# Kernel tuning notes

Hardware: AMD Instinct MI355X
Metric: run time of the kernel (lower is better)

Reference implementation:

```python
import jax, jax.numpy as jnp
import numpy as np

DIM = 1024
N_HEADS = 16
HEAD_DIM = DIM // N_HEADS
SCALE = HEAD_DIM ** (-0.5)


def setup_inputs() -> dict:
    key = jax.random.key(0)
    ks = jax.random.split(key, 5)
    B, N = 2, 2048
    x = jax.random.normal(ks[0], (B, N, DIM), dtype=jnp.float32)
    # torch nn.Linear weight layout: (out_features, in_features)
    qkv_w = jax.random.normal(ks[1], (3 * DIM, DIM), dtype=jnp.float32) * 0.02
    qkv_b = jax.random.normal(ks[2], (3 * DIM,), dtype=jnp.float32) * 0.02
    proj_w = jax.random.normal(ks[3], (DIM, DIM), dtype=jnp.float32) * 0.02
    proj_b = jax.random.normal(ks[4], (DIM,), dtype=jnp.float32) * 0.02
    return {"x": x, "qkv_w": qkv_w, "qkv_b": qkv_b, "proj_w": proj_w, "proj_b": proj_b}


def reference(x, qkv_w, qkv_b, proj_w, proj_b):
    B, N, C = x.shape
    # QKV projection: (B,N,C) -> (B,N,3C)
    qkv = jnp.einsum('bnc,oc->bno', x, qkv_w) + qkv_b
    # (B,N,3,H,Dh) -> (3,B,H,N,Dh)
    qkv = qkv.reshape(B, N, 3, N_HEADS, HEAD_DIM).transpose(2, 0, 3, 1, 4)
    q, k, v = qkv[0], qkv[1], qkv[2]
    attn = jnp.einsum('bhqd,bhkd->bhqk', q, k) * SCALE
    attn = jax.nn.softmax(attn, axis=-1)
    out = jnp.einsum('bhqk,bhkd->bhqd', attn, v)
    out = out.transpose(0, 2, 1, 3).reshape(B, N, C)  # concat heads
    out = jnp.einsum('bnc,oc->bno', out, proj_w) + proj_b
    return out
```

## Files before the change

kernel.cpp:

```cpp
#include <hip/hip_runtime.h>

#define DIM 1024
#define NHEADS 16
#define HD 64
#define NSEQ 2048
#define MROWS 4096
#define QKV_LD 3072

typedef __attribute__((ext_vector_type(8))) short short8;
typedef __attribute__((ext_vector_type(4))) short short4v;
typedef __attribute__((ext_vector_type(4))) float f32x4;

typedef __attribute__((address_space(1))) void gvoid_t;
typedef __attribute__((address_space(3))) void lvoid_t;

#if __has_builtin(__builtin_amdgcn_exp2f)
#define EXP2(x) __builtin_amdgcn_exp2f(x)
#else
#define EXP2(x) exp2f(x)
#endif

#if __has_builtin(__builtin_amdgcn_mfma_f32_16x16x16_bf16)
#define MFMA16(a, b, c) __builtin_amdgcn_mfma_f32_16x16x16_bf16(a, b, c, 0, 0, 0)
#elif __has_builtin(__builtin_amdgcn_mfma_f32_16x16x16bf16_1k)
#define MFMA16(a, b, c) __builtin_amdgcn_mfma_f32_16x16x16bf16_1k(a, b, c, 0, 0, 0)
#else
static __device__ __forceinline__ f32x4 mfma16_asm(short4v a, short4v b, f32x4 c) {
  __asm__("v_mfma_f32_16x16x16_bf16 %0, %1, %2, %0" : "+v"(c) : "v"(a), "v"(b));
  return c;
}
#define MFMA16(a, b, c) mfma16_asm(a, b, c)
#endif

#define EXP_SCALE 0.18033688011112042f

__device__ __forceinline__ unsigned short f2bf(float f) {
  unsigned int u = __builtin_bit_cast(unsigned int, f);
  u += 0x7FFFu + ((u >> 16) & 1u);
  return (unsigned short)(u >> 16);
}

__device__ __forceinline__ void gl_lds16(const void* g, void* l) {
  __builtin_amdgcn_global_load_lds((gvoid_t*)g, (lvoid_t*)l, 16, 0, 0);
}

__global__ __launch_bounds__(256) void cast_bf16_3(
    const float* __restrict__ x, const float* __restrict__ wq,
    const float* __restrict__ wp,
    unsigned short* __restrict__ xb, unsigned short* __restrict__ wqb,
    unsigned short* __restrict__ wpb)
{
  int g = blockIdx.x * 256 + threadIdx.x;
  const float* src;
  unsigned short* dst;
  if (g < 1048576)            { src = x  + (size_t)g * 4;              dst = xb  + (size_t)g * 4; }
  else if (g < 1048576 + 786432) { int t = g - 1048576; src = wq + (size_t)t * 4; dst = wqb + (size_t)t * 4; }
  else                        { int t = g - 1048576 - 786432; src = wp + (size_t)t * 4; dst = wpb + (size_t)t * 4; }
  float4 v = *(const float4*)src;
  ushort4 o;
  o.x = f2bf(v.x); o.y = f2bf(v.y); o.z = f2bf(v.z); o.w = f2bf(v.w);
  *(ushort4*)dst = o;
}

__global__ __launch_bounds__(256) void gemm_nt(
    const unsigned short* __restrict__ A,
    const unsigned short* __restrict__ Bw,
    const float* __restrict__ bias,
    int K, int mode,
    unsigned short* __restrict__ oq,
    unsigned short* __restrict__ ovt,
    float* __restrict__ of)
{
  __shared__ unsigned short As[128 * 32];
  __shared__ unsigned short Bs[128 * 32];

  const int tid  = threadIdx.x;
  const int wave = tid >> 6, lane = tid & 63;
  const int quad = lane >> 4, l15 = lane & 15;
  const int mblk = blockIdx.x * 128;
  const int nblk = blockIdx.y * 128;
  const int wrow = (wave >> 1) * 64, wcol = (wave & 1) * 64;

  f32x4 acc[4][4] = {};

  const int sr = lane >> 2;
  const int sq = (lane & 3) ^ (sr & 3);
  const unsigned short* aBase = A  + (size_t)(mblk + wave * 32 + sr) * K + sq * 8;
  const unsigned short* bBase = Bw + (size_t)(nblk + wave * 32 + sr) * K + sq * 8;

  for (int k0 = 0; k0 < K; k0 += 32) {
    __syncthreads();
    gl_lds16(aBase + k0,          As + (wave * 32) * 32);
    gl_lds16(aBase + 16 * K + k0, As + (wave * 32 + 16) * 32);
    gl_lds16(bBase + k0,          Bs + (wave * 32) * 32);
    gl_lds16(bBase + 16 * K + k0, Bs + (wave * 32 + 16) * 32);
    __syncthreads();

    short8 af[4], bf8[4];
#pragma unroll
    for (int mt = 0; mt < 4; ++mt) {
      int row = wrow + mt * 16 + l15;
      af[mt] = *(const short8*)(As + row * 32 + ((quad ^ (row & 3)) * 8));
    }
#pragma unroll
    for (int nt = 0; nt < 4; ++nt) {
      int row = wcol + nt * 16 + l15;
      bf8[nt] = *(const short8*)(Bs + row * 32 + ((quad ^ (row & 3)) * 8));
    }
#pragma unroll
    for (int mt = 0; mt < 4; ++mt)
#pragma unroll
      for (int nt = 0; nt < 4; ++nt)
        acc[mt][nt] = __builtin_amdgcn_mfma_f32_16x16x32_bf16(af[mt], bf8[nt], acc[mt][nt], 0, 0, 0);
  }

  float bv[4];
#pragma unroll
  for (int nt = 0; nt < 4; ++nt) bv[nt] = bias[nblk + wcol + nt * 16 + l15];

  if (mode == 0) {
#pragma unroll
    for (int mt = 0; mt < 4; ++mt) {
      int row0 = mblk + wrow + mt * 16 + quad * 4;
#pragma unroll
      for (int nt = 0; nt < 4; ++nt) {
        int col = nblk + wcol + nt * 16 + l15;
#pragma unroll
        for (int r = 0; r < 4; ++r)
          of[(size_t)(row0 + r) * DIM + col] = acc[mt][nt][r] + bv[nt];
      }
    }
  } else if (nblk < 2048) {
    const float qs = (nblk < 1024) ? EXP_SCALE : 1.0f;
#pragma unroll
    for (int mt = 0; mt < 4; ++mt) {
      int row0 = mblk + wrow + mt * 16 + quad * 4;
#pragma unroll
      for (int nt = 0; nt < 4; ++nt) {
        int col = nblk + wcol + nt * 16 + l15;
#pragma unroll
        for (int r = 0; r < 4; ++r)
          oq[(size_t)(row0 + r) * QKV_LD + col] = f2bf((acc[mt][nt][r] + bv[nt]) * qs);
      }
    }
  } else {
#pragma unroll
    for (int mt = 0; mt < 4; ++mt) {
      int row0 = mblk + wrow + mt * 16 + quad * 4;
      int n0 = row0 & (NSEQ - 1);
      int bb = row0 >> 11;
      int tt  = n0 >> 6;
      int kin = n0 & 63;
      int kt  = kin >> 4;
      int qv  = (kin >> 2) & 3;
#pragma unroll
      for (int nt = 0; nt < 4; ++nt) {
        int colr = (nblk - 2048) + wcol + nt * 16 + l15;
        int bh = bb * NHEADS + (colr >> 6);
        int d  = colr & 63;
        int dt = d >> 4, dl15 = d & 15;
        ushort4 pk;
        pk.x = f2bf(acc[mt][nt][0] + bv[nt]);
        pk.y = f2bf(acc[mt][nt][1] + bv[nt]);
        pk.z = f2bf(acc[mt][nt][2] + bv[nt]);
        pk.w = f2bf(acc[mt][nt][3] + bv[nt]);
        size_t off = (size_t)(bh * 32 + tt) * 4096 + kt * 1024 + (dt >> 1) * 512
                   + qv * 128 + dl15 * 8 + (dt & 1) * 4;
        *(ushort4*)(ovt + off) = pk;
      }
    }
  }
}

__global__ __launch_bounds__(256) void gemm_nt64(
    const unsigned short* __restrict__ A,
    const unsigned short* __restrict__ Bw,
    const float* __restrict__ bias,
    int K,
    float* __restrict__ of)
{
  __shared__ unsigned short As[64 * 32];
  __shared__ unsigned short Bs[128 * 32];

  const int tid  = threadIdx.x;
  const int wave = tid >> 6, lane = tid & 63;
  const int quad = lane >> 4, l15 = lane & 15;
  const int mblk = blockIdx.x * 64;
  const int nblk = blockIdx.y * 128;
  const int wrow = (wave >> 1) * 32, wcol = (wave & 1) * 64;

  f32x4 acc[2][4] = {};

  const int sr = lane >> 2;
  const int sq = (lane & 3) ^ (sr & 3);
  const unsigned short* aBase = A  + (size_t)(mblk + wave * 16 + sr) * K + sq * 8;
  const unsigned short* bBase = Bw + (size_t)(nblk + wave * 32 + sr) * K + sq * 8;

  for (int k0 = 0; k0 < K; k0 += 32) {
    __syncthreads();
    gl_lds16(aBase + k0,          As + (wave * 16) * 32);
    gl_lds16(bBase + k0,          Bs + (wave * 32) * 32);
    gl_lds16(bBase + 16 * K + k0, Bs + (wave * 32 + 16) * 32);
    __syncthreads();

    short8 af[2], bf8[4];
#pragma unroll
    for (int mt = 0; mt < 2; ++mt) {
      int row = wrow + mt * 16 + l15;
      af[mt] = *(const short8*)(As + row * 32 + ((quad ^ (row & 3)) * 8));
    }
#pragma unroll
    for (int nt = 0; nt < 4; ++nt) {
      int row = wcol + nt * 16 + l15;
      bf8[nt] = *(const short8*)(Bs + row * 32 + ((quad ^ (row & 3)) * 8));
    }
#pragma unroll
    for (int mt = 0; mt < 2; ++mt)
#pragma unroll
      for (int nt = 0; nt < 4; ++nt)
        acc[mt][nt] = __builtin_amdgcn_mfma_f32_16x16x32_bf16(af[mt], bf8[nt], acc[mt][nt], 0, 0, 0);
  }

  float bv[4];
#pragma unroll
  for (int nt = 0; nt < 4; ++nt) bv[nt] = bias[nblk + wcol + nt * 16 + l15];

#pragma unroll
  for (int mt = 0; mt < 2; ++mt) {
    int row0 = mblk + wrow + mt * 16 + quad * 4;
#pragma unroll
    for (int nt = 0; nt < 4; ++nt) {
      int col = nblk + wcol + nt * 16 + l15;
#pragma unroll
      for (int r = 0; r < 4; ++r)
        of[(size_t)(row0 + r) * DIM + col] = acc[mt][nt][r] + bv[nt];
    }
  }
}

__global__ __launch_bounds__(256, 4) void attn_fused(
    const unsigned short* __restrict__ qkv,
    const unsigned short* __restrict__ vfrag,
    unsigned short* __restrict__ aout)
{
  __shared__ unsigned short Ks[2][64 * 64];
  __shared__ unsigned short Vs[2][64 * 64];

  const int tid  = threadIdx.x;
  const int wave = tid >> 6, lane = tid & 63;
  const int quad = lane >> 4, l15 = lane & 15;
  const int bh = blockIdx.x, b = bh >> 4, h = bh & 15;
  const int q0 = blockIdx.y * 64;
  const size_t qkvB = (size_t)b * NSEQ * QKV_LD;

  short8 qf[2];
#pragma unroll
  for (int ks = 0; ks < 2; ++ks)
    qf[ks] = *(const short8*)(qkv + qkvB +
        (size_t)(q0 + wave * 16 + l15) * QKV_LD + h * HD + ks * 32 + quad * 8);

  f32x4 oacc[4] = {};
  float lsum = 0.f;

  const int sr8 = lane >> 3;
  const int sp8 = lane & 7;

  const int r0s = wave * 16 + sr8;
  const int r1s = wave * 16 + 8 + sr8;
  const int qc0 = sp8 ^ (r0s & 7);
  const int qc1 = sp8 ^ (r1s & 7);
  const unsigned short* kBase = qkv + qkvB + DIM + h * HD;
  const unsigned short* kSrc0 = kBase + (size_t)r0s * QKV_LD + qc0 * 8;
  const unsigned short* kSrc1 = kBase + (size_t)r1s * QKV_LD + qc1 * 8;
  const unsigned short* vfT = vfrag + (size_t)bh * 32 * 4096 + wave * 512 + lane * 8;

  auto stage = [&](int bufi, int kkn) {
    gl_lds16(kSrc0 + (size_t)kkn * QKV_LD, &Ks[bufi][(wave * 16) * 64]);
    gl_lds16(kSrc1 + (size_t)kkn * QKV_LD, &Ks[bufi][(wave * 16 + 8) * 64]);
    const unsigned short* vs = vfT + (size_t)(kkn >> 6) * 4096;
    gl_lds16(vs,        &Vs[bufi][wave * 512]);
    gl_lds16(vs + 2048, &Vs[bufi][wave * 512 + 2048]);
  };

  stage(0, 0);
  asm volatile("s_waitcnt vmcnt(0)" ::: "memory");
  __syncthreads();

  for (int kk = 0; kk < NSEQ; kk += 64) {
    const int cur = (kk >> 6) & 1;
    if (kk + 64 < NSEQ) stage(cur ^ 1, kk + 64);

    const unsigned short* Kc = Ks[cur];
    const unsigned short* Vc = Vs[cur];

    short8 kf[4][2];
#pragma unroll
    for (int kt = 0; kt < 4; ++kt)
#pragma unroll
      for (int ks = 0; ks < 2; ++ks) {
        int row = kt * 16 + l15;
        kf[kt][ks] = *(const short8*)(Kc + row * 64 + (((ks * 4 + quad) ^ (row & 7)) * 8));
      }

    f32x4 sacc[4] = {};
    __builtin_amdgcn_s_setprio(1);
#pragma unroll
    for (int kt = 0; kt < 4; ++kt) {
      sacc[kt] = __builtin_amdgcn_mfma_f32_16x16x32_bf16(kf[kt][0], qf[0], sacc[kt], 0, 0, 0);
      sacc[kt] = __builtin_amdgcn_mfma_f32_16x16x32_bf16(kf[kt][1], qf[1], sacc[kt], 0, 0, 0);
    }
    __builtin_amdgcn_s_setprio(0);

    short4v vf[4][4];
#pragma unroll
    for (int kt = 0; kt < 4; ++kt)
#pragma unroll
      for (int p = 0; p < 2; ++p) {
        short8 vv = *(const short8*)(Vc + kt * 1024 + p * 512 + lane * 8);
        vf[2 * p    ][kt] = __builtin_shufflevector(vv, vv, 0, 1, 2, 3);
        vf[2 * p + 1][kt] = __builtin_shufflevector(vv, vv, 4, 5, 6, 7);
      }

#pragma unroll
    for (int kt = 0; kt < 4; ++kt) {
      float p0 = EXP2(sacc[kt][0]);
      float p1 = EXP2(sacc[kt][1]);
      float p2 = EXP2(sacc[kt][2]);
      float p3 = EXP2(sacc[kt][3]);
      lsum += (p0 + p1) + (p2 + p3);
      unsigned r0 = __builtin_bit_cast(unsigned, p0) + 0x8000u;
      unsigned r1 = __builtin_bit_cast(unsigned, p1) + 0x8000u;
      unsigned r2 = __builtin_bit_cast(unsigned, p2) + 0x8000u;
      unsigned r3 = __builtin_bit_cast(unsigned, p3) + 0x8000u;
      uint2 pd;
      pd.x = __builtin_amdgcn_perm(r1, r0, 0x07060302u);
      pd.y = __builtin_amdgcn_perm(r3, r2, 0x07060302u);
      short4v pf = __builtin_bit_cast(short4v, pd);
      __builtin_amdgcn_s_setprio(1);
#pragma unroll
      for (int dt = 0; dt < 4; ++dt)
        oacc[dt] = MFMA16(vf[dt][kt], pf, oacc[dt]);
      __builtin_amdgcn_s_setprio(0);
    }

    asm volatile("s_waitcnt vmcnt(0)" ::: "memory");
    __syncthreads();
  }

  lsum += __shfl_xor(lsum, 16);
  lsum += __shfl_xor(lsum, 32);
  float inv = 1.0f / lsum;

  const int qrow = q0 + wave * 16 + l15;
  const size_t outBase = (size_t)(b * NSEQ + qrow) * DIM + h * HD;
#pragma unroll
  for (int dt = 0; dt < 4; ++dt) {
    unsigned a0 = __builtin_bit_cast(unsigned, oacc[dt][0] * inv) + 0x8000u;
    unsigned a1 = __builtin_bit_cast(unsigned, oacc[dt][1] * inv) + 0x8000u;
    unsigned a2 = __builtin_bit_cast(unsigned, oacc[dt][2] * inv) + 0x8000u;
    unsigned a3 = __builtin_bit_cast(unsigned, oacc[dt][3] * inv) + 0x8000u;
    uint2 st;
    st.x = __builtin_amdgcn_perm(a1, a0, 0x07060302u);
    st.y = __builtin_amdgcn_perm(a3, a2, 0x07060302u);
    *(uint2*)(aout + outBase + dt * 16 + quad * 4) = st;
  }
}

extern "C" void kernel_launch(void* const* d_in, const int* in_sizes, int n_in,
                              void* d_out, int out_size, void* d_ws, size_t ws_size,
                              hipStream_t stream) {
  (void)in_sizes; (void)n_in; (void)out_size; (void)ws_size;
  const float* x      = (const float*)d_in[0];
  const float* qkv_w  = (const float*)d_in[1];
  const float* qkv_b  = (const float*)d_in[2];
  const float* proj_w = (const float*)d_in[3];
  const float* proj_b = (const float*)d_in[4];
  float* out = (float*)d_out;

  char* ws = (char*)d_ws;
  unsigned short* xb   = (unsigned short*)(ws);
  unsigned short* wqb  = (unsigned short*)(ws + ( 8u << 20));
  unsigned short* wpb  = (unsigned short*)(ws + (14u << 20));
  unsigned short* qkv  = (unsigned short*)(ws + (16u << 20));
  unsigned short* vtw  = (unsigned short*)(ws + (40u << 20));
  unsigned short* attn = (unsigned short*)(ws + (48u << 20));

  cast_bf16_3<<<8192, 256, 0, stream>>>(x, qkv_w, proj_w, xb, wqb, wpb);
  gemm_nt<<<dim3(32, 24), 256, 0, stream>>>(xb, wqb, qkv_b, DIM, 1, qkv, vtw, nullptr);
  attn_fused<<<dim3(32, 32), 256, 0, stream>>>(qkv, vtw, attn);
  gemm_nt64<<<dim3(64, 8), 256, 0, stream>>>(attn, wpb, proj_b, DIM, out);
}
```

Baseline: 190.8 us.

## Split attention waves across query and key halves with LDS reduction

Each wave in the fused attention kernel now handles 32 query rows and half of each 64-key tile, instead of 16 query rows and the full tile. Two waves per query half produce partial outputs and partial row sums. At the end these are reduced through shared memory, reusing the K/V buffers, before normalizing and storing. The goal is to read fewer K/V fragments from LDS per MFMA by reusing each K/V fragment across two query sub-tiles. The cost is more accumulator registers, an extra barrier and an LDS reduction at the end.

After: 188.0 us. No clear change (-1.5%).

```diff
diff --git a/kernel.cpp b/kernel.cpp
--- a/kernel.cpp
+++ b/kernel.cpp
@@ -249,18 +249,22 @@
   const int tid  = threadIdx.x;
   const int wave = tid >> 6, lane = tid & 63;
   const int quad = lane >> 4, l15 = lane & 15;
+  const int qh = wave & 1;
+  const int kh = wave >> 1;
   const int bh = blockIdx.x, b = bh >> 4, h = bh & 15;
   const int q0 = blockIdx.y * 64;
   const size_t qkvB = (size_t)b * NSEQ * QKV_LD;
 
-  short8 qf[2];
-#pragma unroll
-  for (int ks = 0; ks < 2; ++ks)
-    qf[ks] = *(const short8*)(qkv + qkvB +
-        (size_t)(q0 + wave * 16 + l15) * QKV_LD + h * HD + ks * 32 + quad * 8);
-
-  f32x4 oacc[4] = {};
-  float lsum = 0.f;
+  short8 qf[2][2];
+#pragma unroll
+  for (int nq = 0; nq < 2; ++nq)
+#pragma unroll
+    for (int ks = 0; ks < 2; ++ks)
+      qf[nq][ks] = *(const short8*)(qkv + qkvB +
+          (size_t)(q0 + qh * 32 + nq * 16 + l15) * QKV_LD + h * HD + ks * 32 + quad * 8);
+
+  f32x4 oacc[4][2] = {};
+  float lsum[2] = {0.f, 0.f};
 
   const int sr8 = lane >> 3;
   const int sp8 = lane & 7;
@@ -293,76 +297,116 @@
     const unsigned short* Kc = Ks[cur];
     const unsigned short* Vc = Vs[cur];
 
-    short8 kf[4][2];
-#pragma unroll
-    for (int kt = 0; kt < 4; ++kt)
+    short8 kf[2][2];
+#pragma unroll
+    for (int kt = 0; kt < 2; ++kt)
 #pragma unroll
       for (int ks = 0; ks < 2; ++ks) {
-        int row = kt * 16 + l15;
+        int row = kh * 32 + kt * 16 + l15;
         kf[kt][ks] = *(const short8*)(Kc + row * 64 + (((ks * 4 + quad) ^ (row & 7)) * 8));
       }
 
-    f32x4 sacc[4] = {};
+    f32x4 sacc[2][2] = {};
     __builtin_amdgcn_s_setprio(1);
 #pragma unroll
-    for (int kt = 0; kt < 4; ++kt) {
-      sacc[kt] = __builtin_amdgcn_mfma_f32_16x16x32_bf16(kf[kt][0], qf[0], sacc[kt], 0, 0, 0);
-      sacc[kt] = __builtin_amdgcn_mfma_f32_16x16x32_bf16(kf[kt][1], qf[1], sacc[kt], 0, 0, 0);
-    }
+    for (int kt = 0; kt < 2; ++kt)
+#pragma unroll
+      for (int nq = 0; nq < 2; ++nq) {
+        sacc[kt][nq] = __builtin_amdgcn_mfma_f32_16x16x32_bf16(kf[kt][0], qf[nq][0], sacc[kt][nq], 0, 0, 0);
+        sacc[kt][nq] = __builtin_amdgcn_mfma_f32_16x16x32_bf16(kf[kt][1], qf[nq][1], sacc[kt][nq], 0, 0, 0);
+      }
     __builtin_amdgcn_s_setprio(0);
 
-    short4v vf[4][4];
-#pragma unroll
-    for (int kt = 0; kt < 4; ++kt)
+    short4v vf[4][2];
+#pragma unroll
+    for (int kt = 0; kt < 2; ++kt)
 #pragma unroll
       for (int p = 0; p < 2; ++p) {
-        short8 vv = *(const short8*)(Vc + kt * 1024 + p * 512 + lane * 8);
+        short8 vv = *(const short8*)(Vc + (kh * 2 + kt) * 1024 + p * 512 + lane * 8);
         vf[2 * p    ][kt] = __builtin_shufflevector(vv, vv, 0, 1, 2, 3);
         vf[2 * p + 1][kt] = __builtin_shufflevector(vv, vv, 4, 5, 6, 7);
       }
 
 #pragma unroll
-    for (int kt = 0; kt < 4; ++kt) {
-      float p0 = EXP2(sacc[kt][0]);
-      float p1 = EXP2(sacc[kt][1]);
-      float p2 = EXP2(sacc[kt][2]);
-      float p3 = EXP2(sacc[kt][3]);
-      lsum += (p0 + p1) + (p2 + p3);
-      unsigned r0 = __builtin_bit_cast(unsigned, p0) + 0x8000u;
-      unsigned r1 = __builtin_bit_cast(unsigned, p1) + 0x8000u;
-      unsigned r2 = __builtin_bit_cast(unsigned, p2) + 0x8000u;
-      unsigned r3 = __builtin_bit_cast(unsigned, p3) + 0x8000u;
-      uint2 pd;
-      pd.x = __builtin_amdgcn_perm(r1, r0, 0x07060302u);
-      pd.y = __builtin_amdgcn_perm(r3, r2, 0x07060302u);
-      short4v pf = __builtin_bit_cast(short4v, pd);
-      __builtin_amdgcn_s_setprio(1);
+    for (int kt = 0; kt < 2; ++kt)
+#pragma unroll
+      for (int nq = 0; nq < 2; ++nq) {
+        float p0 = EXP2(sacc[kt][nq][0]);
+        float p1 = EXP2(sacc[kt][nq][1]);
+        float p2 = EXP2(sacc[kt][nq][2]);
+        float p3 = EXP2(sacc[kt][nq][3]);
+        lsum[nq] += (p0 + p1) + (p2 + p3);
+        unsigned r0 = __builtin_bit_cast(unsigned, p0) + 0x8000u;
+        unsigned r1 = __builtin_bit_cast(unsigned, p1) + 0x8000u;
+        unsigned r2 = __builtin_bit_cast(unsigned, p2) + 0x8000u;
+        unsigned r3 = __builtin_bit_cast(unsigned, p3) + 0x8000u;
+        uint2 pd;
+        pd.x = __builtin_amdgcn_perm(r1, r0, 0x07060302u);
+        pd.y = __builtin_amdgcn_perm(r3, r2, 0x07060302u);
+        short4v pf = __builtin_bit_cast(short4v, pd);
+        __builtin_amdgcn_s_setprio(1);
+#pragma unroll
+        for (int dt = 0; dt < 4; ++dt)
+          oacc[dt][nq] = MFMA16(vf[dt][kt], pf, oacc[dt][nq]);
+        __builtin_amdgcn_s_setprio(0);
+      }
+
+    asm volatile("s_waitcnt vmcnt(0)" ::: "memory");
+    __syncthreads();
+  }
+
+#pragma unroll
+  for (int nq = 0; nq < 2; ++nq) {
+    lsum[nq] += __shfl_xor(lsum[nq], 16);
+    lsum[nq] += __shfl_xor(lsum[nq], 32);
+  }
+
+  {
+    float* red0 = (float*)&Ks[0][0];
+    float* red1 = (float*)&Vs[0][0];
+    float* red = qh ? red1 : red0;
+    const int base = lane * 34;
+    if (kh == 1) {
 #pragma unroll
       for (int dt = 0; dt < 4; ++dt)
-        oacc[dt] = MFMA16(vf[dt][kt], pf, oacc[dt]);
-      __builtin_amdgcn_s_setprio(0);
-    }
-
-    asm volatile("s_waitcnt vmcnt(0)" ::: "memory");
-    __syncthreads();
-  }
-
-  lsum += __shfl_xor(lsum, 16);
-  lsum += __shfl_xor(lsum, 32);
-  float inv = 1.0f / lsum;
-
-  const int qrow = q0 + wave * 16 + l15;
-  const size_t outBase = (size_t)(b * NSEQ + qrow) * DIM + h * HD;
-#pragma unroll
-  for (int dt = 0; dt < 4; ++dt) {
-    unsigned a0 = __builtin_bit_cast(unsigned, oacc[dt][0] * inv) + 0x8000u;
-    unsigned a1 = __builtin_bit_cast(unsigned, oacc[dt][1] * inv) + 0x8000u;
-    unsigned a2 = __builtin_bit_cast(unsigned, oacc[dt][2] * inv) + 0x8000u;
-    unsigned a3 = __builtin_bit_cast(unsigned, oacc[dt][3] * inv) + 0x8000u;
-    uint2 st;
-    st.x = __builtin_amdgcn_perm(a1, a0, 0x07060302u);
-    st.y = __builtin_amdgcn_perm(a3, a2, 0x07060302u);
-    *(uint2*)(aout + outBase + dt * 16 + quad * 4) = st;
+#pragma unroll
+        for (int nq = 0; nq < 2; ++nq)
+#pragma unroll
+          for (int r = 0; r < 4; ++r)
+            red[base + dt * 8 + nq * 4 + r] = oacc[dt][nq][r];
+      red[base + 32] = lsum[0];
+      red[base + 33] = lsum[1];
+    }
+    __syncthreads();
+    if (kh == 0) {
+#pragma unroll
+      for (int dt = 0; dt < 4; ++dt)
+#pragma unroll
+        for (int nq = 0; nq < 2; ++nq)
+#pragma unroll
+          for (int r = 0; r < 4; ++r)
+            oacc[dt][nq][r] += red[base + dt * 8 + nq * 4 + r];
+      lsum[0] += red[base + 32];
+      lsum[1] += red[base + 33];
+
+      const size_t outB = (size_t)(b * NSEQ + q0 + qh * 32) * DIM + h * HD;
+#pragma unroll
+      for (int nq = 0; nq < 2; ++nq) {
+        float inv = 1.0f / lsum[nq];
+        const size_t rowB = outB + (size_t)(nq * 16 + l15) * DIM;
+#pragma unroll
+        for (int dt = 0; dt < 4; ++dt) {
+          unsigned a0 = __builtin_bit_cast(unsigned, oacc[dt][nq][0] * inv) + 0x8000u;
+          unsigned a1 = __builtin_bit_cast(unsigned, oacc[dt][nq][1] * inv) + 0x8000u;
+          unsigned a2 = __builtin_bit_cast(unsigned, oacc[dt][nq][2] * inv) + 0x8000u;
+          unsigned a3 = __builtin_bit_cast(unsigned, oacc[dt][nq][3] * inv) + 0x8000u;
+          uint2 st;
+          st.x = __builtin_amdgcn_perm(a1, a0, 0x07060302u);
+          st.y = __builtin_amdgcn_perm(a3, a2, 0x07060302u);
+          *(uint2*)(aout + rowB + dt * 16 + quad * 4) = st;
+        }
+      }
+    }
   }
 }
 
```

## Split attention key range across wave pairs with LDS reduction, direct V loads

Applied to the files above, without the earlier changes.

Each attention block now covers 32 query rows instead of 64. The four waves form two query halves times two key halves, and each wave processes 32 of the 64 keys per tile. V fragments are read straight from global memory into registers instead of being staged through LDS. A final LDS reduction merges the partial outputs and row sums of the two key halves. The grid doubles, and launch bounds rise to 6 blocks per CU to raise parallelism and occupancy, at the cost of an extra reduction, a barrier, and more K traffic per query.

New measurement: 199.4 us. +4.5%, slower.

```diff
diff --git a/kernel.cpp b/kernel.cpp
--- a/kernel.cpp
+++ b/kernel.cpp
@@ -238,26 +238,27 @@
   }
 }
 
-__global__ __launch_bounds__(256, 4) void attn_fused(
+__global__ __launch_bounds__(256, 6) void attn_fused(
     const unsigned short* __restrict__ qkv,
     const unsigned short* __restrict__ vfrag,
     unsigned short* __restrict__ aout)
 {
   __shared__ unsigned short Ks[2][64 * 64];
-  __shared__ unsigned short Vs[2][64 * 64];
 
   const int tid  = threadIdx.x;
   const int wave = tid >> 6, lane = tid & 63;
   const int quad = lane >> 4, l15 = lane & 15;
+  const int qh = wave & 1;
+  const int kh = wave >> 1;
   const int bh = blockIdx.x, b = bh >> 4, h = bh & 15;
-  const int q0 = blockIdx.y * 64;
+  const int q0 = blockIdx.y * 32;
   const size_t qkvB = (size_t)b * NSEQ * QKV_LD;
 
   short8 qf[2];
 #pragma unroll
   for (int ks = 0; ks < 2; ++ks)
     qf[ks] = *(const short8*)(qkv + qkvB +
-        (size_t)(q0 + wave * 16 + l15) * QKV_LD + h * HD + ks * 32 + quad * 8);
+        (size_t)(q0 + qh * 16 + l15) * QKV_LD + h * HD + ks * 32 + quad * 8);
 
   f32x4 oacc[4] = {};
   float lsum = 0.f;
@@ -272,57 +273,61 @@
   const unsigned short* kBase = qkv + qkvB + DIM + h * HD;
   const unsigned short* kSrc0 = kBase + (size_t)r0s * QKV_LD + qc0 * 8;
   const unsigned short* kSrc1 = kBase + (size_t)r1s * QKV_LD + qc1 * 8;
-  const unsigned short* vfT = vfrag + (size_t)bh * 32 * 4096 + wave * 512 + lane * 8;
-
-  auto stage = [&](int bufi, int kkn) {
+  const unsigned short* vfT = vfrag + (size_t)bh * 32 * 4096 + lane * 8;
+
+  auto stageK = [&](int bufi, int kkn) {
     gl_lds16(kSrc0 + (size_t)kkn * QKV_LD, &Ks[bufi][(wave * 16) * 64]);
     gl_lds16(kSrc1 + (size_t)kkn * QKV_LD, &Ks[bufi][(wave * 16 + 8) * 64]);
-    const unsigned short* vs = vfT + (size_t)(kkn >> 6) * 4096;
-    gl_lds16(vs,        &Vs[bufi][wave * 512]);
-    gl_lds16(vs + 2048, &Vs[bufi][wave * 512 + 2048]);
   };
 
-  stage(0, 0);
+  stageK(0, 0);
   asm volatile("s_waitcnt vmcnt(0)" ::: "memory");
   __syncthreads();
 
   for (int kk = 0; kk < NSEQ; kk += 64) {
     const int cur = (kk >> 6) & 1;
-    if (kk + 64 < NSEQ) stage(cur ^ 1, kk + 64);
-
-    const unsigned short* Kc = Ks[cur];
-    const unsigned short* Vc = Vs[cur];
-
-    short8 kf[4][2];
-#pragma unroll
-    for (int kt = 0; kt < 4; ++kt)
+    if (kk + 64 < NSEQ) stageK(cur ^ 1, kk + 64);
+
+    const unsigned short* vt = vfT + (size_t)(kk >> 6) * 4096 + kh * 2048;
+    short8 vv[4];
+#pragma unroll
+    for (int kt = 0; kt < 2; ++kt)
+#pragma unroll
+      for (int p = 0; p < 2; ++p)
+        vv[kt * 2 + p] = *(const short8*)(vt + kt * 1024 + p * 512);
+
+    const unsigned short* Kc = &Ks[cur][0];
+
+    short8 kf[2][2];
+#pragma unroll
+    for (int kt = 0; kt < 2; ++kt)
 #pragma unroll
       for (int ks = 0; ks < 2; ++ks) {
-        int row = kt * 16 + l15;
+        int row = kh * 32 + kt * 16 + l15;
         kf[kt][ks] = *(const short8*)(Kc + row * 64 + (((ks * 4 + quad) ^ (row & 7)) * 8));
       }
 
-    f32x4 sacc[4] = {};
+    f32x4 sacc[2] = {};
     __builtin_amdgcn_s_setprio(1);
 #pragma unroll
-    for (int kt = 0; kt < 4; ++kt) {
+    for (int kt = 0; kt < 2; ++kt) {
       sacc[kt] = __builtin_amdgcn_mfma_f32_16x16x32_bf16(kf[kt][0], qf[0], sacc[kt], 0, 0, 0);
       sacc[kt] = __builtin_amdgcn_mfma_f32_16x16x32_bf16(kf[kt][1], qf[1], sacc[kt], 0, 0, 0);
     }
     __builtin_amdgcn_s_setprio(0);
 
-    short4v vf[4][4];
-#pragma unroll
-    for (int kt = 0; kt < 4; ++kt)
+    short4v vf[4][2];
+#pragma unroll
+    for (int kt = 0; kt < 2; ++kt)
 #pragma unroll
       for (int p = 0; p < 2; ++p) {
-        short8 vv = *(const short8*)(Vc + kt * 1024 + p * 512 + lane * 8);
-        vf[2 * p    ][kt] = __builtin_shufflevector(vv, vv, 0, 1, 2, 3);
-        vf[2 * p + 1][kt] = __builtin_shufflevector(vv, vv, 4, 5, 6, 7);
-      }
-
-#pragma unroll
-    for (int kt = 0; kt < 4; ++kt) {
+        short8 v8 = vv[kt * 2 + p];
+        vf[2 * p    ][kt] = __builtin_shufflevector(v8, v8, 0, 1, 2, 3);
+        vf[2 * p + 1][kt] = __builtin_shufflevector(v8, v8, 4, 5, 6, 7);
+      }
+
+#pragma unroll
+    for (int kt = 0; kt < 2; ++kt) {
       float p0 = EXP2(sacc[kt][0]);
       float p1 = EXP2(sacc[kt][1]);
       float p2 = EXP2(sacc[kt][2]);
@@ -349,20 +354,42 @@
 
   lsum += __shfl_xor(lsum, 16);
   lsum += __shfl_xor(lsum, 32);
-  float inv = 1.0f / lsum;
-
-  const int qrow = q0 + wave * 16 + l15;
-  const size_t outBase = (size_t)(b * NSEQ + qrow) * DIM + h * HD;
-#pragma unroll
-  for (int dt = 0; dt < 4; ++dt) {
-    unsigned a0 = __builtin_bit_cast(unsigned, oacc[dt][0] * inv) + 0x8000u;
-    unsigned a1 = __builtin_bit_cast(unsigned, oacc[dt][1] * inv) + 0x8000u;
-    unsigned a2 = __builtin_bit_cast(unsigned, oacc[dt][2] * inv) + 0x8000u;
-    unsigned a3 = __builtin_bit_cast(unsigned, oacc[dt][3] * inv) + 0x8000u;
-    uint2 st;
-    st.x = __builtin_amdgcn_perm(a1, a0, 0x07060302u);
-    st.y = __builtin_amdgcn_perm(a3, a2, 0x07060302u);
-    *(uint2*)(aout + outBase + dt * 16 + quad * 4) = st;
+
+  {
+    float* redf = (float*)&Ks[0][0];
+    float* red = redf + qh * 1152;
+    const int base = lane * 18;
+    if (kh == 1) {
+#pragma unroll
+      for (int dt = 0; dt < 4; ++dt)
+#pragma unroll
+        for (int r = 0; r < 4; ++r)
+          red[base + dt * 4 + r] = oacc[dt][r];
+      red[base + 16] = lsum;
+    }
+    __syncthreads();
+    if (kh == 0) {
+#pragma unroll
+      for (int dt = 0; dt < 4; ++dt)
+#pragma unroll
+        for (int r = 0; r < 4; ++r)
+          oacc[dt][r] += red[base + dt * 4 + r];
+      lsum += red[base + 16];
+
+      float inv = 1.0f / lsum;
+      const size_t rowB = (size_t)(b * NSEQ + q0 + qh * 16 + l15) * DIM + h * HD;
+#pragma unroll
+      for (int dt = 0; dt < 4; ++dt) {
+        unsigned a0 = __builtin_bit_cast(unsigned, oacc[dt][0] * inv) + 0x8000u;
+        unsigned a1 = __builtin_bit_cast(unsigned, oacc[dt][1] * inv) + 0x8000u;
+        unsigned a2 = __builtin_bit_cast(unsigned, oacc[dt][2] * inv) + 0x8000u;
+        unsigned a3 = __builtin_bit_cast(unsigned, oacc[dt][3] * inv) + 0x8000u;
+        uint2 st;
+        st.x = __builtin_amdgcn_perm(a1, a0, 0x07060302u);
+        st.y = __builtin_amdgcn_perm(a3, a2, 0x07060302u);
+        *(uint2*)(aout + rowB + dt * 16 + quad * 4) = st;
+      }
+    }
   }
 }
 
@@ -387,6 +414,6 @@
 
   cast_bf16_3<<<8192, 256, 0, stream>>>(x, qkv_w, proj_w, xb, wqb, wpb);
   gemm_nt<<<dim3(32, 24), 256, 0, stream>>>(xb, wqb, qkv_b, DIM, 1, qkv, vtw, nullptr);
-  attn_fused<<<dim3(32, 32), 256, 0, stream>>>(qkv, vtw, attn);
+  attn_fused<<<dim3(32, 64), 256, 0, stream>>>(qkv, vtw, attn);
   gemm_nt64<<<dim3(64, 8), 256, 0, stream>>>(attn, wpb, proj_b, DIM, out);
 }
```
